# Kernel optimization log

Hardware: AMD Instinct MI355X
Metric: run time of the kernel (lower is better)

The kernel has to match this reference:

```python
import jax, jax.numpy as jnp
import numpy as np

BLOCK = 8      # block_size
HALO = 3       # halo_size
WIN = BLOCK + 2 * HALO   # 14, kv window size
NH = 8         # num_heads
DH = 32        # dim_head
DIM = 256
DIM_QK = NH * DH          # 256
DV = 256                  # dim_v = dim_out
DVH = DV // NH            # 32
SCALE = DH ** -0.5
REL = 2 * WIN - 1         # 27


def rel_logits_1d(q, rel_k, permute_mask):
    # q: (B, H, W, d); rel_k: (rel_size, d)
    B, H, W, d = q.shape
    rel_size = rel_k.shape[0]
    win = (rel_size + 1) // 2
    x = jnp.einsum('bhwd,rd->bhwr', q, rel_k).reshape(-1, W, rel_size)
    # skew trick: pad + reshape turns absolute into relative indexing
    x = jnp.pad(x, ((0, 0), (0, 0), (0, 1))).reshape(x.shape[0], -1)
    x = jnp.pad(x, ((0, 0), (0, rel_size - W))).reshape(-1, W + 1, rel_size)
    x = x[:, :W, win - 1:]
    x = jnp.broadcast_to(x.reshape(B, H, 1, W, win), (B, H, win, W, win))
    return jnp.transpose(x, permute_mask)


def pos_embed_rel(q, height_rel, width_rel):
    # q: (B*NH, num_blocks, block*block, DH)
    B, BB, HW, dh = q.shape
    q4 = q.reshape(-1, BLOCK, BLOCK, dh)
    rel_w = rel_logits_1d(q4, width_rel, (0, 1, 3, 2, 4))
    rel_h = rel_logits_1d(jnp.transpose(q4, (0, 2, 1, 3)), height_rel, (0, 3, 1, 4, 2))
    return (rel_h + rel_w).reshape(B, BB, HW, -1)


def setup_inputs() -> dict:
    key = jax.random.key(0)
    k1, k2, k3, k4, k5 = jax.random.split(key, 5)
    B, H, W = 4, 128, 128
    std = DIM ** -0.5
    return {
        'x': jax.random.normal(k1, (B, DIM, H, W), dtype=jnp.float32),
        'w_q': jax.random.normal(k2, (DIM_QK, DIM), dtype=jnp.float32) * std,
        'w_kv': jax.random.normal(k3, (DIM_QK + DV, DIM), dtype=jnp.float32) * std,
        'height_rel': jax.random.normal(k4, (REL, DH), dtype=jnp.float32) * SCALE,
        'width_rel': jax.random.normal(k5, (REL, DH), dtype=jnp.float32) * SCALE,
    }


def reference(x, w_q, w_kv, height_rel, width_rel):
    B, C, H, W = x.shape
    nhb, nwb = H // BLOCK, W // BLOCK
    nb = nhb * nwb
    # 1x1 convs as matmuls over channel dim
    q = jnp.einsum('bchw,oc->bohw', x, w_q)
    q = q.reshape(B * NH, DH, nhb, BLOCK, nwb, BLOCK)
    q = jnp.transpose(q, (0, 1, 3, 5, 2, 4)).reshape(B * NH, DH, BLOCK * BLOCK, nb)
    q = jnp.transpose(q, (0, 3, 2, 1))              # (B*NH, nb, bs^2, DH)

    kv = jnp.einsum('bchw,oc->bohw', x, w_kv)
    kv = jnp.pad(kv, ((0, 0), (0, 0), (HALO, HALO), (HALO, HALO)))
    ih = jnp.arange(nhb)[:, None] * BLOCK + jnp.arange(WIN)[None, :]
    iw = jnp.arange(nwb)[:, None] * BLOCK + jnp.arange(WIN)[None, :]
    kv = kv[:, :, ih]
    kv = kv[:, :, :, :, iw]
    kv = jnp.transpose(kv, (0, 1, 2, 4, 3, 5))
    kv = kv.reshape(B * NH, DH + DVH, nb, WIN * WIN)
    kv = jnp.transpose(kv, (0, 2, 3, 1))
    k, v = kv[..., :DH], kv[..., DH:]

    logits = jnp.einsum('bnqd,bnkd->bnqk', q, k) * SCALE
    logits = logits + pos_embed_rel(q, height_rel, width_rel)
    attn = jax.nn.softmax(logits, axis=-1)
    out = jnp.einsum('bnqk,bnkd->bnqd', attn, v)    # (B*NH, nb, bs^2, DVH)
    out = jnp.transpose(out, (0, 3, 2, 1))          # (B*NH, DVH, bs^2, nb)
    out = out.reshape(-1, BLOCK, BLOCK, nhb, nwb)
    out = jnp.transpose(out, (0, 3, 1, 4, 2)).reshape(B, DV, H, W)
    return out
```

## Files before the change

### kernel.cpp

```cpp
#include <hip/hip_runtime.h>
#include <stdint.h>


typedef short bf16s;
typedef bf16s bf16x8 __attribute__((ext_vector_type(8)));
typedef float f32x4  __attribute__((ext_vector_type(4)));
typedef unsigned int u32x4 __attribute__((ext_vector_type(4)));

#define MFMA16(a, b, c) __builtin_amdgcn_mfma_f32_16x16x32_bf16(a, b, c, 0, 0, 0)
#define SCALE_QK 0.17677669529663687f
#define LOG2E 1.4426950408889634f
#define EXP_SHIFT 11.541560327111707f

__device__ __forceinline__ void async16(void* lds, const void* g) {
  __builtin_amdgcn_global_load_lds(
      (const __attribute__((address_space(1))) unsigned int*)g,
      (__attribute__((address_space(3))) unsigned int*)lds, 16, 0, 0);
}

__device__ __forceinline__ bf16s f2b(float f) {
  unsigned int u = __builtin_bit_cast(unsigned int, f);
  u = (u + 0x7fffu + ((u >> 16) & 1u)) >> 16;
  return (bf16s)u;
}

__global__ __launch_bounds__(256) void k_convert(const float* __restrict__ wq,
                                                 const float* __restrict__ wkv,
                                                 const float* __restrict__ hrel,
                                                 const float* __restrict__ wrel,
                                                 bf16s* __restrict__ wq_b,
                                                 bf16s* __restrict__ wkv_b,
                                                 bf16s* __restrict__ rel_b) {
  int i = blockIdx.x * 256 + threadIdx.x;
  if (i < 65536) {
    wq_b[i] = f2b(wq[i]);
  } else if (i < 196608) {
    int j = i - 65536;
    wkv_b[j] = f2b(wkv[j]);
  } else {
    int r2 = i - 196608;
    int relid = r2 >> 10, r = (r2 >> 5) & 31, d = r2 & 31;
    const float* src = relid ? hrel : wrel;
    rel_b[r2] = (r < 27) ? f2b(src[r * 32 + d]) : (bf16s)0;
  }
}

__global__ __launch_bounds__(256) void k_transpose(const float* __restrict__ x,
                                                   bf16s* __restrict__ xT) {
  __shared__ bf16s tile[64][72];
  const int ct = blockIdx.x, pt = blockIdx.y, b = blockIdx.z;
  const int t = threadIdx.x;
  const int r0 = t >> 3, c8 = (t & 7) * 8;
  const float* src = x + ((size_t)b * 256 + ct * 64) * 16384 + (size_t)pt * 64;
#pragma unroll
  for (int pass = 0; pass < 2; ++pass) {
    int r = pass * 32 + r0;
    const float4* sp = (const float4*)(src + (size_t)r * 16384 + c8);
    float4 f0 = sp[0], f1 = sp[1];
    bf16x8 v;
    v[0] = f2b(f0.x); v[1] = f2b(f0.y); v[2] = f2b(f0.z); v[3] = f2b(f0.w);
    v[4] = f2b(f1.x); v[5] = f2b(f1.y); v[6] = f2b(f1.z); v[7] = f2b(f1.w);
    *(bf16x8*)&tile[r][c8] = v;
  }
  __syncthreads();
  bf16s* dst = xT + ((size_t)b * 16384 + pt * 64) * 256 + ct * 64;
#pragma unroll
  for (int pass = 0; pass < 2; ++pass) {
    int p = pass * 32 + r0;
    bf16x8 v;
#pragma unroll
    for (int u = 0; u < 8; ++u) v[u] = tile[c8 + u][p];
    *(bf16x8*)(dst + (size_t)p * 256 + c8) = v;
  }
}

__global__ __launch_bounds__(256) void k_zero_border(bf16s* __restrict__ kv) {
  const int gid = blockIdx.x * 256 + threadIdx.x;
  const int chunk = gid & 63;
  const int rest = gid >> 6;
  const int b = rest / 1572, pxi = rest % 1572;
  int y, x;
  if (pxi < 804) {
    int r = pxi / 134;
    x = pxi % 134;
    y = (r < 3) ? r : 128 + r;
  } else {
    int p2 = pxi - 804;
    y = 3 + p2 / 6;
    int xi = p2 % 6;
    x = (xi < 3) ? xi : 128 + xi;
  }
  u32x4 z = {0, 0, 0, 0};
  *(u32x4*)(kv + (((size_t)b * 134 + y) * 134 + x) * 512 + chunk * 8) = z;
}

__global__ __launch_bounds__(256) void k_qkv(const bf16s* __restrict__ wq,
                                             const bf16s* __restrict__ wkv,
                                             const bf16s* __restrict__ xT,
                                             bf16s* __restrict__ q_ws,
                                             bf16s* __restrict__ kv_ws) {
  __shared__ __align__(16) bf16s smem[17408];
  bf16s* Al = smem;
  bf16s* Bl = smem + 4096;
  const int mt = blockIdx.x, y = blockIdx.y, b = blockIdx.z;
  const int t = threadIdx.x;
  const int wv = t >> 6, lane = t & 63, g = lane >> 4, l15 = lane & 15;
  const int wm = wv & 1, wn = wv >> 1;
  const bf16s* Ag = (mt < 2) ? (wq + mt * 128 * 256) : (wkv + (mt - 2) * 128 * 256);
  const bf16s* Bg = xT + ((size_t)b * 16384 + y * 128) * 256;

  f32x4 acc[4][4];
#pragma unroll
  for (int i = 0; i < 4; ++i)
#pragma unroll
    for (int j = 0; j < 4; ++j) acc[i][j] = (f32x4){0.f, 0.f, 0.f, 0.f};

  for (int kc = 0; kc < 8; ++kc) {
    __syncthreads();
#pragma unroll
    for (int hh = 0; hh < 2; ++hh) {
      int tt = hh * 256 + t;
      int row = tt >> 2, k8 = (tt & 3) * 8;
      async16((char*)Al + hh * 4096 + wv * 1024, Ag + row * 256 + kc * 32 + k8);
      async16((char*)Bl + hh * 4096 + wv * 1024, Bg + row * 256 + kc * 32 + k8);
    }
    __syncthreads();
    bf16x8 af[4], bfr[4];
#pragma unroll
    for (int mi = 0; mi < 4; ++mi)
      af[mi] = *(const bf16x8*)&Al[(wm * 64 + mi * 16 + l15) * 32 + g * 8];
#pragma unroll
    for (int ni = 0; ni < 4; ++ni)
      bfr[ni] = *(const bf16x8*)&Bl[(wn * 64 + ni * 16 + l15) * 32 + g * 8];
#pragma unroll
    for (int mi = 0; mi < 4; ++mi)
#pragma unroll
      for (int ni = 0; ni < 4; ++ni)
        acc[mi][ni] = MFMA16(af[mi], bfr[ni], acc[mi][ni]);
  }

  __syncthreads();
  bf16s* Cl = smem;
#pragma unroll
  for (int mi = 0; mi < 4; ++mi)
#pragma unroll
    for (int ni = 0; ni < 4; ++ni)
#pragma unroll
      for (int rg = 0; rg < 4; ++rg) {
        int m = wm * 64 + mi * 16 + g * 4 + rg;
        int n = wn * 64 + ni * 16 + l15;
        Cl[n * 136 + m] = f2b(acc[mi][ni][rg]);
      }
  __syncthreads();

  if (mt < 2) {
#pragma unroll
    for (int hh = 0; hh < 2; ++hh) {
      int rid = hh * 256 + t;
      int head = rid >> 7, bx = (rid >> 3) & 15, wc = rid & 7;
      int px = bx * 8 + wc;
      bf16s* dst = q_ws +
          ((((size_t)(b * 8 + mt * 4 + head) * 256 + (y >> 3) * 16 + bx) * 64 +
            (y & 7) * 8 + wc)) * 32;
#pragma unroll
      for (int c4 = 0; c4 < 4; ++c4)
        *(bf16x8*)(dst + c4 * 8) = *(const bf16x8*)&Cl[px * 136 + head * 32 + c4 * 8];
    }
  } else {
    int px = t >> 1, half = t & 1;
    bf16s* dst = kv_ws + (((size_t)b * 134 + y + 3) * 134 + px + 3) * 512 +
                 (mt - 2) * 128 + half * 64;
#pragma unroll
    for (int c8 = 0; c8 < 8; ++c8)
      *(bf16x8*)(dst + c8 * 8) = *(const bf16x8*)&Cl[px * 136 + half * 64 + c8 * 8];
  }
}

__global__ __launch_bounds__(256, 3) void k_attn(const bf16s* __restrict__ q_ws,
                                                 const bf16s* __restrict__ kv_ws,
                                                 const bf16s* __restrict__ rel_b,
                                                 float* __restrict__ outp) {
  __shared__ __align__(16) char arena[43008];
  bf16s* vT = (bf16s*)arena;
  const int t = threadIdx.x;
  const int wv = t >> 6, lane = t & 63, g = lane >> 4, l15 = lane & 15;
  char* pw = arena + 14336 + wv * 7168;
  float* RWp = (float*)pw;
  float* RHp = RWp + 544;
  bf16s* pP  = (bf16s*)pw;

  int wgid = blockIdx.x;
  int xcd = wgid & 7, chnk = wgid >> 3;
  int bxlo = chnk & 3, rest = chnk >> 2;
  int c = xcd * 256 + rest;
  int bx = (c & 3) * 4 + bxlo;
  int byy = (c >> 2) & 15;
  int bh = c >> 6;
  int b = bh >> 3, hd = bh & 7;
  int blk = byy * 16 + bx;

  const bf16s* kvb = kv_ws + (((size_t)b * 134 + byy * 8) * 134 + bx * 8) * 512 + hd * 64;
  const bf16s* qg  = q_ws + ((size_t)bh * 256 + blk) * 2048;

  bf16x8 aq = *(const bf16x8*)(qg + (wv * 16 + l15) * 32 + g * 8);
  const int i_cl = (l15 < 14) ? l15 : 13;
  const bf16s* kbase = kvb + (size_t)i_cl * 68608 + g * 8;
  bf16x8 kf[14];
#pragma unroll
  for (int nt = 0; nt < 14; ++nt)
    kf[nt] = *(const bf16x8*)(kbase + nt * 512);
  bf16x8 wf[2], hf[2];
#pragma unroll
  for (int t16 = 0; t16 < 2; ++t16) {
    wf[t16] = *(const bf16x8*)(rel_b + (t16 * 16 + l15) * 32 + g * 8);
    hf[t16] = *(const bf16x8*)(rel_b + 1024 + (t16 * 16 + l15) * 32 + g * 8);
  }

  for (int idx = t; idx < 784; idx += 256) {
    int pos = idx >> 2, ch = idx & 3;
    int i = pos / 14, j = pos - i * 14;
    bf16x8 v = *(const bf16x8*)(kvb + (size_t)(i * 134 + j) * 512 + 32 + ch * 8);
#pragma unroll
    for (int u = 0; u < 8; ++u) vT[(ch * 8 + u) * 224 + j * 16 + i] = v[u];
  }
  for (int idx = t; idx < 896; idx += 256) {
    int d = idx / 28, r = idx - d * 28;
    vT[d * 224 + (r >> 1) * 16 + 14 + (r & 1)] = 0;
  }

  f32x4 acc[14];
#pragma unroll
  for (int nt = 0; nt < 14; ++nt) acc[nt] = (f32x4){0.f, 0.f, 0.f, 0.f};
#pragma unroll
  for (int nt = 0; nt < 14; ++nt) acc[nt] = MFMA16(kf[nt], aq, acc[nt]);

  {
    f32x4 zz = (f32x4){0.f, 0.f, 0.f, 0.f};
#pragma unroll
    for (int t16 = 0; t16 < 2; ++t16) {
      f32x4 rw = MFMA16(wf[t16], aq, zz);
      f32x4 rh = MFMA16(hf[t16], aq, zz);
#pragma unroll
      for (int rg = 0; rg < 4; ++rg) {
        RWp[l15 * 34 + t16 * 16 + g * 4 + rg] = rw[rg];
        RHp[l15 * 34 + t16 * 16 + g * 4 + rg] = rh[rg];
      }
    }
  }

  const int jq = l15 & 7;
  const int iq = wv * 2 + (l15 >> 3);
  const float* RWr = RWp + l15 * 34;
  const float* RHr = RHp + l15 * 34;
  const int ihb = 13 + g * 4 - iq;
  float h0 = RHr[ihb], h1 = RHr[ihb + 1], h2 = RHr[ihb + 2], h3 = RHr[ihb + 3];
  float sm = 0.f;
#pragma unroll
  for (int nt = 0; nt < 14; ++nt) {
    float w1 = RWr[13 + nt - jq];
    float e0 = exp2f(fmaf(fmaf(acc[nt][0], SCALE_QK, w1 + h0), LOG2E, -EXP_SHIFT));
    float e1 = exp2f(fmaf(fmaf(acc[nt][1], SCALE_QK, w1 + h1), LOG2E, -EXP_SHIFT));
    float e2 = exp2f(fmaf(fmaf(acc[nt][2], SCALE_QK, w1 + h2), LOG2E, -EXP_SHIFT));
    float e3 = exp2f(fmaf(fmaf(acc[nt][3], SCALE_QK, w1 + h3), LOG2E, -EXP_SHIFT));
    if (g == 3) { e2 = 0.f; e3 = 0.f; }
    sm += e0 + e1 + e2 + e3;
    acc[nt][0] = e0; acc[nt][1] = e1; acc[nt][2] = e2; acc[nt][3] = e3;
  }
  sm += __shfl_xor(sm, 16);
  sm += __shfl_xor(sm, 32);
  float rs = __builtin_amdgcn_rcpf(sm);

#pragma unroll
  for (int nt = 0; nt < 14; ++nt) {
    bf16s p0 = f2b(acc[nt][0] * rs), p1 = f2b(acc[nt][1] * rs);
    bf16s p2 = f2b(acc[nt][2] * rs), p3 = f2b(acc[nt][3] * rs);
    unsigned int lo = (unsigned short)p0 | ((unsigned int)(unsigned short)p1 << 16);
    unsigned int hi = (unsigned short)p2 | ((unsigned int)(unsigned short)p3 << 16);
    *(uint2*)(pP + l15 * 224 + nt * 16 + g * 4) = make_uint2(lo, hi);
  }

  __syncthreads();

  f32x4 oa0 = (f32x4){0.f, 0.f, 0.f, 0.f};
  f32x4 oa1 = (f32x4){0.f, 0.f, 0.f, 0.f};
#pragma unroll
  for (int ks = 0; ks < 7; ++ks) {
    bf16x8 bp = *(const bf16x8*)(pP + l15 * 224 + ks * 32 + g * 8);
    bf16x8 a0 = *(const bf16x8*)(vT + l15 * 224 + ks * 32 + g * 8);
    bf16x8 a1 = *(const bf16x8*)(vT + (16 + l15) * 224 + ks * 32 + g * 8);
    oa0 = MFMA16(a0, bp, oa0);
    oa1 = MFMA16(a1, bp, oa1);
  }

  {
    int py = wv * 2 + (l15 >> 3), px = l15 & 7;
    float* ob = outp + (((size_t)(b * 256 + hd * 32) * 128 + byy * 8 + py) * 128) +
                bx * 8 + px;
#pragma unroll
    for (int rg = 0; rg < 4; ++rg) {
      ob[(size_t)(g * 4 + rg) * 16384] = oa0[rg];
      ob[(size_t)(16 + g * 4 + rg) * 16384] = oa1[rg];
    }
  }
}

extern "C" void kernel_launch(void* const* d_in, const int* in_sizes, int n_in,
                              void* d_out, int out_size, void* d_ws, size_t ws_size,
                              hipStream_t stream) {
  (void)in_sizes; (void)n_in; (void)out_size; (void)ws_size;
  const float* x    = (const float*)d_in[0];
  const float* wq   = (const float*)d_in[1];
  const float* wkv  = (const float*)d_in[2];
  const float* hrel = (const float*)d_in[3];
  const float* wrel = (const float*)d_in[4];
  float* outp = (float*)d_out;

  bf16s* xT    = (bf16s*)d_ws;
  bf16s* q_ws  = xT + 16777216;
  bf16s* kv_ws = q_ws + 16777216;
  bf16s* wq_b  = kv_ws + 36773888;
  bf16s* wkv_b = wq_b + 65536;
  bf16s* rel_b = wkv_b + 131072;

  hipLaunchKernelGGL(k_convert,    dim3(776),       dim3(256), 0, stream,
                     wq, wkv, hrel, wrel, wq_b, wkv_b, rel_b);
  hipLaunchKernelGGL(k_transpose,  dim3(4, 256, 4), dim3(256), 0, stream, x, xT);
  hipLaunchKernelGGL(k_zero_border, dim3(1572),     dim3(256), 0, stream, kv_ws);
  hipLaunchKernelGGL(k_qkv,        dim3(6, 128, 4), dim3(256), 0, stream,
                     wq_b, wkv_b, xT, q_ws, kv_ws);
  hipLaunchKernelGGL(k_attn,       dim3(8192),      dim3(256), 0, stream,
                     q_ws, kv_ws, rel_b, outp);
}
```

Before: 300.7 us.

## Split K and V workspaces, store V channel-major for direct vT staging

The combined kv workspace is split into a pixel-major K buffer and a channel-major padded V buffer. k_qkv writes V transposed, using alignbit to handle the odd 11-element offset, so k_attn can fill its vT tile with vectorized copies instead of scalar LDS transposes. The LDS layouts of P and V gain an XOR swizzle to avoid bank conflicts. The softmax now folds the width terms into precomputed per-lane constants and uses the native exp2, and the output is written with float4 stores. The cost is an extra LDS staging pass in k_qkv, more complex border zeroing, and strided K reads that now span rows.

Result: no change. 302.6 us (+0.6%).

```diff
diff --git a/kernel.cpp b/kernel.cpp
--- a/kernel.cpp
+++ b/kernel.cpp
@@ -74,31 +74,48 @@
   }
 }
 
-__global__ __launch_bounds__(256) void k_zero_border(bf16s* __restrict__ kv) {
+__global__ __launch_bounds__(256) void k_zero_border(bf16s* __restrict__ kvK,
+                                                     bf16s* __restrict__ vws) {
   const int gid = blockIdx.x * 256 + threadIdx.x;
-  const int chunk = gid & 63;
-  const int rest = gid >> 6;
-  const int b = rest / 1572, pxi = rest % 1572;
-  int y, x;
-  if (pxi < 804) {
-    int r = pxi / 134;
-    x = pxi % 134;
-    y = (r < 3) ? r : 128 + r;
+  u32x4 z = {0, 0, 0, 0};
+  if (gid < 201216) {
+    int chunk = gid & 31;
+    int pxid = gid >> 5;
+    int b = pxid / 1572, pxi = pxid % 1572;
+    int y, x;
+    if (pxi < 804) {
+      int r = pxi / 134;
+      x = pxi % 134;
+      y = (r < 3) ? r : 128 + r;
+    } else {
+      int p2 = pxi - 804;
+      y = 3 + p2 / 6;
+      int xi = p2 % 6;
+      x = (xi < 3) ? xi : 128 + xi;
+    }
+    *(u32x4*)(kvK + (((size_t)b * 134 + y) * 134 + x) * 256 + chunk * 8) = z;
+  } else if (gid < 311808) {
+    int idx = gid - 201216;
+    int plane = idx / 108, r = idx - plane * 108;
+    int row6 = r / 18, c8 = (r - row6 * 18) * 8;
+    int y = (row6 < 3) ? row6 : 128 + row6;
+    *(u32x4*)(vws + ((size_t)plane * 134 + y) * 144 + c8) = z;
   } else {
-    int p2 = pxi - 804;
-    y = 3 + p2 / 6;
-    int xi = p2 % 6;
-    x = (xi < 3) ? xi : 128 + xi;
-  }
-  u32x4 z = {0, 0, 0, 0};
-  *(u32x4*)(kv + (((size_t)b * 134 + y) * 134 + x) * 512 + chunk * 8) = z;
+    int idx = gid - 311808;
+    int plane = idx >> 8, r = idx & 255;
+    int y = 3 + (r >> 1);
+    bf16s* row = vws + ((size_t)plane * 134 + y) * 144;
+    if (r & 1) { row[139] = 0; *(unsigned int*)(row + 140) = 0; }
+    else       { *(unsigned int*)(row + 8) = 0; row[10] = 0; }
+  }
 }
 
 __global__ __launch_bounds__(256) void k_qkv(const bf16s* __restrict__ wq,
                                              const bf16s* __restrict__ wkv,
                                              const bf16s* __restrict__ xT,
                                              bf16s* __restrict__ q_ws,
-                                             bf16s* __restrict__ kv_ws) {
+                                             bf16s* __restrict__ kv_K,
+                                             bf16s* __restrict__ v_ws) {
   __shared__ __align__(16) bf16s smem[17408];
   bf16s* Al = smem;
   bf16s* Bl = smem + 4096;
@@ -140,20 +157,19 @@
   }
 
   __syncthreads();
-  bf16s* Cl = smem;
-#pragma unroll
-  for (int mi = 0; mi < 4; ++mi)
-#pragma unroll
-    for (int ni = 0; ni < 4; ++ni)
-#pragma unroll
-      for (int rg = 0; rg < 4; ++rg) {
-        int m = wm * 64 + mi * 16 + g * 4 + rg;
-        int n = wn * 64 + ni * 16 + l15;
-        Cl[n * 136 + m] = f2b(acc[mi][ni][rg]);
-      }
-  __syncthreads();
-
   if (mt < 2) {
+    bf16s* Cl = smem;
+#pragma unroll
+    for (int mi = 0; mi < 4; ++mi)
+#pragma unroll
+      for (int ni = 0; ni < 4; ++ni)
+#pragma unroll
+        for (int rg = 0; rg < 4; ++rg) {
+          int m = wm * 64 + mi * 16 + g * 4 + rg;
+          int n = wn * 64 + ni * 16 + l15;
+          Cl[n * 136 + m] = f2b(acc[mi][ni][rg]);
+        }
+    __syncthreads();
 #pragma unroll
     for (int hh = 0; hh < 2; ++hh) {
       int rid = hh * 256 + t;
@@ -167,17 +183,71 @@
         *(bf16x8*)(dst + c4 * 8) = *(const bf16x8*)&Cl[px * 136 + head * 32 + c4 * 8];
     }
   } else {
-    int px = t >> 1, half = t & 1;
-    bf16s* dst = kv_ws + (((size_t)b * 134 + y + 3) * 134 + px + 3) * 512 +
-                 (mt - 2) * 128 + half * 64;
-#pragma unroll
-    for (int c8 = 0; c8 < 8; ++c8)
-      *(bf16x8*)(dst + c8 * 8) = *(const bf16x8*)&Cl[px * 136 + half * 64 + c8 * 8];
+    bf16s* Cl = smem;
+#pragma unroll
+    for (int mi = 0; mi < 4; ++mi)
+#pragma unroll
+      for (int ni = 0; ni < 4; ++ni)
+#pragma unroll
+        for (int rg = 0; rg < 4; ++rg) {
+          int m = wm * 64 + mi * 16 + g * 4 + rg;
+          int n = wn * 64 + ni * 16 + l15;
+          Cl[n * 136 + m] = f2b(acc[mi][ni][rg]);
+        }
+    __syncthreads();
+    {
+      int px = t >> 1, sel = t & 1;
+      int head = 2 * (mt - 2) + sel;
+      bf16s* dst = kv_K + (((size_t)b * 134 + y + 3) * 134 + px + 3) * 256 + head * 32;
+#pragma unroll
+      for (int c4 = 0; c4 < 4; ++c4)
+        *(bf16x8*)(dst + c4 * 8) = *(const bf16x8*)&Cl[px * 136 + sel * 64 + c4 * 8];
+    }
+    __syncthreads();
+    bf16s* ClV = smem;
+#pragma unroll
+    for (int mi = 0; mi < 4; ++mi)
+#pragma unroll
+      for (int ni = 0; ni < 4; ++ni)
+#pragma unroll
+        for (int rg = 0; rg < 4; ++rg) {
+          int m = wm * 64 + mi * 16 + g * 4 + rg;
+          int n = wn * 64 + ni * 16 + l15;
+          ClV[m * 132 + n] = f2b(acc[mi][ni][rg]);
+        }
+    __syncthreads();
+    {
+      int vrow = t >> 2, q2 = t & 3;
+      int hsel = vrow >> 5, d = vrow & 31;
+      int o_local = 32 + d + hsel * 64;
+      int head = 2 * (mt - 2) + hsel;
+      bf16s* gv = v_ws +
+          (((size_t)(b * 8 + head) * 32 + d) * 134 + (y + 3)) * 144 + 11 + q2 * 32;
+      unsigned int dws[16];
+#pragma unroll
+      for (int u = 0; u < 8; ++u) {
+        uint2 rr = *(const uint2*)&ClV[o_local * 132 + q2 * 32 + u * 4];
+        dws[2 * u] = rr.x;
+        dws[2 * u + 1] = rr.y;
+      }
+      gv[0] = (bf16s)(dws[0] & 0xffffu);
+#pragma unroll
+      for (int j = 0; j < 7; ++j) {
+        uint2 w;
+        w.x = __builtin_amdgcn_alignbit(dws[2 * j + 1], dws[2 * j], 16);
+        w.y = __builtin_amdgcn_alignbit(dws[2 * j + 2], dws[2 * j + 1], 16);
+        *(uint2*)(gv + 1 + 4 * j) = w;
+      }
+      *(unsigned int*)(gv + 29) =
+          __builtin_amdgcn_alignbit(dws[15], dws[14], 16);
+      gv[31] = (bf16s)(dws[15] >> 16);
+    }
   }
 }
 
 __global__ __launch_bounds__(256, 3) void k_attn(const bf16s* __restrict__ q_ws,
-                                                 const bf16s* __restrict__ kv_ws,
+                                                 const bf16s* __restrict__ kv_K,
+                                                 const bf16s* __restrict__ v_ws,
                                                  const bf16s* __restrict__ rel_b,
                                                  float* __restrict__ outp) {
   __shared__ __align__(16) char arena[43008];
@@ -199,33 +269,28 @@
   int b = bh >> 3, hd = bh & 7;
   int blk = byy * 16 + bx;
 
-  const bf16s* kvb = kv_ws + (((size_t)b * 134 + byy * 8) * 134 + bx * 8) * 512 + hd * 64;
-  const bf16s* qg  = q_ws + ((size_t)bh * 256 + blk) * 2048;
-
+  for (int idx = t; idx < 1792; idx += 256) {
+    int d = idx / 56, r = idx - d * 56;
+    int i = r >> 2, q4 = r & 3;
+    uint2 val = *(const uint2*)(v_ws +
+        (((size_t)(bh * 32 + d)) * 134 + byy * 8 + i) * 144 + bx * 8 + 8 + q4 * 4);
+    *(uint2*)&vT[d * 224 + (((i * 4 + q4) ^ (d & 7)) << 2)] = val;
+  }
+
+  const bf16s* qg = q_ws + ((size_t)bh * 256 + blk) * 2048;
   bf16x8 aq = *(const bf16x8*)(qg + (wv * 16 + l15) * 32 + g * 8);
-  const int i_cl = (l15 < 14) ? l15 : 13;
-  const bf16s* kbase = kvb + (size_t)i_cl * 68608 + g * 8;
+  const int jcl = (l15 < 14) ? l15 : 13;
+  const bf16s* kbase = kv_K +
+      (((size_t)b * 134 + byy * 8) * 134 + bx * 8 + jcl) * 256 + hd * 32 + g * 8;
   bf16x8 kf[14];
 #pragma unroll
   for (int nt = 0; nt < 14; ++nt)
-    kf[nt] = *(const bf16x8*)(kbase + nt * 512);
+    kf[nt] = *(const bf16x8*)(kbase + (size_t)nt * 34304);
   bf16x8 wf[2], hf[2];
 #pragma unroll
   for (int t16 = 0; t16 < 2; ++t16) {
     wf[t16] = *(const bf16x8*)(rel_b + (t16 * 16 + l15) * 32 + g * 8);
     hf[t16] = *(const bf16x8*)(rel_b + 1024 + (t16 * 16 + l15) * 32 + g * 8);
-  }
-
-  for (int idx = t; idx < 784; idx += 256) {
-    int pos = idx >> 2, ch = idx & 3;
-    int i = pos / 14, j = pos - i * 14;
-    bf16x8 v = *(const bf16x8*)(kvb + (size_t)(i * 134 + j) * 512 + 32 + ch * 8);
-#pragma unroll
-    for (int u = 0; u < 8; ++u) vT[(ch * 8 + u) * 224 + j * 16 + i] = v[u];
-  }
-  for (int idx = t; idx < 896; idx += 256) {
-    int d = idx / 28, r = idx - d * 28;
-    vT[d * 224 + (r >> 1) * 16 + 14 + (r & 1)] = 0;
   }
 
   f32x4 acc[14];
@@ -252,16 +317,20 @@
   const int iq = wv * 2 + (l15 >> 3);
   const float* RWr = RWp + l15 * 34;
   const float* RHr = RHp + l15 * 34;
-  const int ihb = 13 + g * 4 - iq;
-  float h0 = RHr[ihb], h1 = RHr[ihb + 1], h2 = RHr[ihb + 2], h3 = RHr[ihb + 3];
+  const int iwb = 13 + g * 4 - jq;
+  float wL0 = fmaf(RWr[iwb],     LOG2E, -EXP_SHIFT);
+  float wL1 = fmaf(RWr[iwb + 1], LOG2E, -EXP_SHIFT);
+  float wL2 = fmaf(RWr[iwb + 2], LOG2E, -EXP_SHIFT);
+  float wL3 = fmaf(RWr[iwb + 3], LOG2E, -EXP_SHIFT);
+  const float SL = SCALE_QK * LOG2E;
   float sm = 0.f;
 #pragma unroll
   for (int nt = 0; nt < 14; ++nt) {
-    float w1 = RWr[13 + nt - jq];
-    float e0 = exp2f(fmaf(fmaf(acc[nt][0], SCALE_QK, w1 + h0), LOG2E, -EXP_SHIFT));
-    float e1 = exp2f(fmaf(fmaf(acc[nt][1], SCALE_QK, w1 + h1), LOG2E, -EXP_SHIFT));
-    float e2 = exp2f(fmaf(fmaf(acc[nt][2], SCALE_QK, w1 + h2), LOG2E, -EXP_SHIFT));
-    float e3 = exp2f(fmaf(fmaf(acc[nt][3], SCALE_QK, w1 + h3), LOG2E, -EXP_SHIFT));
+    float hL = RHr[13 + nt - iq] * LOG2E;
+    float e0 = __builtin_amdgcn_exp2f(fmaf(acc[nt][0], SL, wL0 + hL));
+    float e1 = __builtin_amdgcn_exp2f(fmaf(acc[nt][1], SL, wL1 + hL));
+    float e2 = __builtin_amdgcn_exp2f(fmaf(acc[nt][2], SL, wL2 + hL));
+    float e3 = __builtin_amdgcn_exp2f(fmaf(acc[nt][3], SL, wL3 + hL));
     if (g == 3) { e2 = 0.f; e3 = 0.f; }
     sm += e0 + e1 + e2 + e3;
     acc[nt][0] = e0; acc[nt][1] = e1; acc[nt][2] = e2; acc[nt][3] = e3;
@@ -270,13 +339,14 @@
   sm += __shfl_xor(sm, 32);
   float rs = __builtin_amdgcn_rcpf(sm);
 
+  const int s = l15 & 7;
 #pragma unroll
   for (int nt = 0; nt < 14; ++nt) {
     bf16s p0 = f2b(acc[nt][0] * rs), p1 = f2b(acc[nt][1] * rs);
     bf16s p2 = f2b(acc[nt][2] * rs), p3 = f2b(acc[nt][3] * rs);
     unsigned int lo = (unsigned short)p0 | ((unsigned int)(unsigned short)p1 << 16);
     unsigned int hi = (unsigned short)p2 | ((unsigned int)(unsigned short)p3 << 16);
-    *(uint2*)(pP + l15 * 224 + nt * 16 + g * 4) = make_uint2(lo, hi);
+    *(uint2*)(pP + l15 * 224 + (((nt * 4 + g) ^ s) << 2)) = make_uint2(lo, hi);
   }
 
   __syncthreads();
@@ -285,22 +355,29 @@
   f32x4 oa1 = (f32x4){0.f, 0.f, 0.f, 0.f};
 #pragma unroll
   for (int ks = 0; ks < 7; ++ks) {
-    bf16x8 bp = *(const bf16x8*)(pP + l15 * 224 + ks * 32 + g * 8);
-    bf16x8 a0 = *(const bf16x8*)(vT + l15 * 224 + ks * 32 + g * 8);
-    bf16x8 a1 = *(const bf16x8*)(vT + (16 + l15) * 224 + ks * 32 + g * 8);
-    oa0 = MFMA16(a0, bp, oa0);
-    oa1 = MFMA16(a1, bp, oa1);
+    int G0 = ks * 8 + g * 2, G1 = G0 + 1;
+    uint2 pa = *(const uint2*)(pP + l15 * 224 + ((G0 ^ s) << 2));
+    uint2 pb = *(const uint2*)(pP + l15 * 224 + ((G1 ^ s) << 2));
+    u32x4 ap4 = {pa.x, pa.y, pb.x, pb.y};
+    bf16x8 ap = __builtin_bit_cast(bf16x8, ap4);
+    uint2 va = *(const uint2*)(vT + l15 * 224 + ((G0 ^ s) << 2));
+    uint2 vb = *(const uint2*)(vT + l15 * 224 + ((G1 ^ s) << 2));
+    u32x4 b04 = {va.x, va.y, vb.x, vb.y};
+    bf16x8 bv0 = __builtin_bit_cast(bf16x8, b04);
+    uint2 vc = *(const uint2*)(vT + (16 + l15) * 224 + ((G0 ^ s) << 2));
+    uint2 vd = *(const uint2*)(vT + (16 + l15) * 224 + ((G1 ^ s) << 2));
+    u32x4 b14 = {vc.x, vc.y, vd.x, vd.y};
+    bf16x8 bv1 = __builtin_bit_cast(bf16x8, b14);
+    oa0 = MFMA16(ap, bv0, oa0);
+    oa1 = MFMA16(ap, bv1, oa1);
   }
 
   {
-    int py = wv * 2 + (l15 >> 3), px = l15 & 7;
-    float* ob = outp + (((size_t)(b * 256 + hd * 32) * 128 + byy * 8 + py) * 128) +
-                bx * 8 + px;
-#pragma unroll
-    for (int rg = 0; rg < 4; ++rg) {
-      ob[(size_t)(g * 4 + rg) * 16384] = oa0[rg];
-      ob[(size_t)(16 + g * 4 + rg) * 16384] = oa1[rg];
-    }
+    size_t base = (((size_t)(b * 256 + hd * 32 + l15) * 128 +
+                    byy * 8 + wv * 2 + (g >> 1)) * 128) + bx * 8 + (g & 1) * 4;
+    *(float4*)(outp + base) = make_float4(oa0[0], oa0[1], oa0[2], oa0[3]);
+    *(float4*)(outp + base + (size_t)16 * 16384) =
+        make_float4(oa1[0], oa1[1], oa1[2], oa1[3]);
   }
 }
 
@@ -317,17 +394,18 @@
 
   bf16s* xT    = (bf16s*)d_ws;
   bf16s* q_ws  = xT + 16777216;
-  bf16s* kv_ws = q_ws + 16777216;
-  bf16s* wq_b  = kv_ws + 36773888;
+  bf16s* kv_K  = q_ws + 16777216;
+  bf16s* v_ws  = kv_K + 18386944;
+  bf16s* wq_b  = v_ws + 19759104;
   bf16s* wkv_b = wq_b + 65536;
   bf16s* rel_b = wkv_b + 131072;
 
   hipLaunchKernelGGL(k_convert,    dim3(776),       dim3(256), 0, stream,
                      wq, wkv, hrel, wrel, wq_b, wkv_b, rel_b);
   hipLaunchKernelGGL(k_transpose,  dim3(4, 256, 4), dim3(256), 0, stream, x, xT);
-  hipLaunchKernelGGL(k_zero_border, dim3(1572),     dim3(256), 0, stream, kv_ws);
+  hipLaunchKernelGGL(k_zero_border, dim3(2242),     dim3(256), 0, stream, kv_K, v_ws);
   hipLaunchKernelGGL(k_qkv,        dim3(6, 128, 4), dim3(256), 0, stream,
-                     wq_b, wkv_b, xT, q_ws, kv_ws);
+                     wq_b, wkv_b, xT, q_ws, kv_K, v_ws);
   hipLaunchKernelGGL(k_attn,       dim3(8192),      dim3(256), 0, stream,
-                     q_ws, kv_ws, rel_b, outp);
-}
+                     q_ws, kv_K, v_ws, rel_b, outp);
+}
```
